# Kernel optimization log

Measured on AMD Instinct MI355X. Metric: run time of the kernel, lower is better.

The kernel has to match this reference:

```python
import jax, jax.numpy as jnp
import numpy as np

N = 8192          # total genes
B = 16            # number of ragged batch groups (equal-size here: 512 each)
D = 768           # hidden_dim
NEG = -1.0e9      # mask fill value used by the original module


def setup_inputs() -> dict:
    key = jax.random.key(0)
    ks = jax.random.split(key, 10)
    s = 0.02
    inp = {
        "gene_embeddings": jax.random.normal(ks[0], (N, D), dtype=jnp.float32),
        # sorted group ids: 16 contiguous groups of 512 genes
        "batch": (jnp.arange(N) // (N // B)).astype(jnp.int64),
        "Wq": jax.random.normal(ks[1], (D, D), dtype=jnp.float32) * s,
        "bq": jnp.zeros((D,), dtype=jnp.float32),
        "Wk": jax.random.normal(ks[2], (D, D), dtype=jnp.float32) * s,
        "bk": jnp.zeros((D,), dtype=jnp.float32),
        "Wv": jax.random.normal(ks[3], (D, D), dtype=jnp.float32) * s,
        "bv": jnp.zeros((D,), dtype=jnp.float32),
        "Wo": jax.random.normal(ks[4], (D, D), dtype=jnp.float32) * s,
        "bo": jnp.zeros((D,), dtype=jnp.float32),
        "beta": jnp.ones((1,), dtype=jnp.float32) * 0.1,
    }
    return inp


def reference(gene_embeddings, batch, Wq, bq, Wk, bk, Wv, bv, Wo, bo, beta):
    # Single-head attention over full hidden_dim (num_heads unused in original).
    x = gene_embeddings
    q = x @ Wq.T + bq                      # [N, D]
    k = x @ Wk.T + bk
    v = x @ Wv.T + bv
    scale = 1.0 / jnp.sqrt(jnp.asarray(D, dtype=x.dtype))
    scores = (q @ k.T) * scale             # [N, N]
    # block-diagonal group mask + diagonal self-mask (same -1e9 fill as torch code)
    same_group = batch[:, None] == batch[None, :]
    eye = jnp.eye(N, dtype=bool)
    allow = same_group & (~eye)
    scores = jnp.where(allow, scores, NEG)
    weights = jax.nn.softmax(scores, axis=-1)   # dropout in eval mode -> identity
    dyn = weights @ v                       # [N, D]
    dyn = dyn @ Wo.T + bo
    return x + beta * dyn
```

## Files before the change

### kernel.cpp

```cpp
#include <hip/hip_runtime.h>
#include <hip/hip_bf16.h>
#include <cstdint>

using u16 = unsigned short;
using u32 = unsigned int;

typedef __bf16 bf16x8 __attribute__((ext_vector_type(8)));
typedef float  f32x4  __attribute__((ext_vector_type(4)));

__device__ __forceinline__ u32 f2b2(float a, float b) {
    __hip_bfloat162 h = __float22bfloat162_rn(float2{a, b});
    u32 u;
    __builtin_memcpy(&u, &h, 4);
    return u;
}
__device__ __forceinline__ float b2f(u16 b) {
    u32 u = (u32)b << 16;
    float f;
    __builtin_memcpy(&f, &u, 4);
    return f;
}

__device__ __forceinline__ void gload_lds16(const u16* g, u16* l) {
    __builtin_amdgcn_global_load_lds(
        (const __attribute__((address_space(1))) void*)g,
        (__attribute__((address_space(3))) void*)l,
        16, 0, 0);
}

#define VMCNT(N)  asm volatile("s_waitcnt vmcnt(" #N ")" ::: "memory")
#define LGKMCNT0  asm volatile("s_waitcnt lgkmcnt(0)" ::: "memory")
#define BARRIER   asm volatile("s_barrier" ::: "memory")

__launch_bounds__(256)
__global__ void pack_kernel(const float* __restrict__ x,
                            const float* __restrict__ Wq,
                            const float* __restrict__ Wk,
                            const float* __restrict__ Wv,
                            const float* __restrict__ Wo,
                            const float* __restrict__ bq,
                            const float* __restrict__ bv,
                            const float* __restrict__ bo,
                            u16* __restrict__ xb,
                            u16* __restrict__ Wob,
                            u16* __restrict__ WqT,
                            u16* __restrict__ WkT,
                            u16* __restrict__ WvT,
                            float* __restrict__ czk,
                            float* __restrict__ bvoo)
{
    __shared__ u16 tl[64][72];
    const int b = blockIdx.x, tid = threadIdx.x;

    if (b < 3360) {
        int c = b * 256 + tid;
        long e = (long)c * 8;
        const float* src; u16* dst; long off;
        if (e < 6291456L) { src = x;  dst = xb;  off = e; }
        else              { src = Wo; dst = Wob; off = e - 6291456L; }
        float4 v0 = *(const float4*)(src + off);
        float4 v1 = *(const float4*)(src + off + 4);
        uint4 o;
        o.x = f2b2(v0.x, v0.y); o.y = f2b2(v0.z, v0.w);
        o.z = f2b2(v1.x, v1.y); o.w = f2b2(v1.z, v1.w);
        *(uint4*)(dst + off) = o;
    } else if (b < 3792) {
        int t = b - 3360;
        int w = t / 144, tt = t % 144;
        int tr = tt / 12, tc = tt % 12;
        const float* src0 = (w == 0) ? Wq : (w == 1) ? Wk : Wv;
        u16* dst0 = (w == 0) ? WqT : (w == 1) ? WkT : WvT;
        int lr = tid >> 2, lcb = (tid & 3) * 16;
        const float* src = src0 + (long)(tr * 64 + lr) * 768 + tc * 64 + lcb;
#pragma unroll
        for (int q = 0; q < 4; q++) {
            float4 v = *(const float4*)(src + q * 4);
            u32 p0 = f2b2(v.x, v.y), p1 = f2b2(v.z, v.w);
            tl[lr][lcb + q * 4 + 0] = (u16)p0;
            tl[lr][lcb + q * 4 + 1] = (u16)(p0 >> 16);
            tl[lr][lcb + q * 4 + 2] = (u16)p1;
            tl[lr][lcb + q * 4 + 3] = (u16)(p1 >> 16);
        }
        __syncthreads();
        int li = tid >> 2, lkb = (tid & 3) * 16;
        u16 o[16];
#pragma unroll
        for (int j = 0; j < 16; j++) o[j] = tl[lkb + j][li];
        u16* dst = dst0 + (long)(tc * 64 + li) * 768 + tr * 64 + lkb;
#pragma unroll
        for (int j = 0; j < 16; j++) dst[j] = o[j];
    } else if (b < 3984) {
        int wave = tid >> 6, lane = tid & 63;
        int j = (b - 3792) * 4 + wave;
        float acc = 0.f;
#pragma unroll
        for (int i = 0; i < 12; i++) {
            int rr = i * 64 + lane;
            acc += Wk[(long)rr * 768 + j] * bq[rr];
        }
#pragma unroll
        for (int d = 32; d; d >>= 1) acc += __shfl_xor(acc, d);
        if (lane == 0) czk[j] = acc;
    } else {
        int wave = tid >> 6, lane = tid & 63;
        int j = (b - 3984) * 4 + wave;
        float acc = 0.f;
#pragma unroll
        for (int i = 0; i < 12; i++) {
            int k = i * 64 + lane;
            acc += Wo[(long)j * 768 + k] * bv[k];
        }
#pragma unroll
        for (int d = 32; d; d >>= 1) acc += __shfl_xor(acc, d);
        if (lane == 0) bvoo[j] = acc + bo[j];
    }
}

template<int TM, int TN, int MODE>
__device__ __forceinline__ void gemm_body(
        const u16* __restrict__ A, int lda, long sAz,
        const u16* __restrict__ B, int ldb, long sBz,
        void* __restrict__ Cv, int ldc, long sCz,
        int K,
        const float* __restrict__ bias,
        float scale,
        u16* __restrict__ vTout)
{
    constexpr int FI = TM / 32;
    constexpr int FJ = TN / 32;
    constexpr int CA = TM / 64;
    constexpr int CB = TN / 64;

    __shared__ u16 As[2][TM * 32];
    __shared__ u16 Bs[2][TN * 32];

    const int tid  = threadIdx.x;
    const int g    = blockIdx.z;
    const u16* Ab = A + (long)g * sAz + (long)blockIdx.y * TM * lda;
    const u16* Bb = B + (long)g * sBz + (long)blockIdx.x * TN * ldb;

    const int wave = tid >> 6, lane = tid & 63;
    const int wm = (wave >> 1) * (TM / 2), wn = (wave & 1) * (TN / 2);
    const int ln15 = lane & 15, lq = lane >> 4;

    f32x4 acc[FI][FJ];
#pragma unroll
    for (int i = 0; i < FI; i++)
#pragma unroll
        for (int j = 0; j < FJ; j++)
            acc[i][j] = (f32x4){0.f, 0.f, 0.f, 0.f};

    const int srow = lane >> 2;
    const int sc   = ((lane & 3) ^ ((lane >> 4) & 3)) * 8;
    const u16* Ag[CA]; const u16* Bg[CB];
    int Al[CA], Bl[CB];
#pragma unroll
    for (int t = 0; t < CA; t++) {
        int c = wave * CA + t;
        Ag[t] = Ab + (long)(c * 16 + srow) * lda + sc;
        Al[t] = c * 512;
    }
#pragma unroll
    for (int t = 0; t < CB; t++) {
        int c = wave * CB + t;
        Bg[t] = Bb + (long)(c * 16 + srow) * ldb + sc;
        Bl[t] = c * 512;
    }

    const int foff = ln15 * 32 + ((lq ^ (ln15 >> 2)) * 8);
    const int nk = K >> 5;

#pragma unroll
    for (int t = 0; t < CA; t++) gload_lds16(Ag[t], &As[0][Al[t]]);
#pragma unroll
    for (int t = 0; t < CB; t++) gload_lds16(Bg[t], &Bs[0][Bl[t]]);

    for (int kt = 0; kt < nk; kt++) {
        const int cur = kt & 1;
        __syncthreads();
        if (kt + 1 < nk) {
            const int k0 = (kt + 1) * 32, nxt = cur ^ 1;
#pragma unroll
            for (int t = 0; t < CA; t++) gload_lds16(Ag[t] + k0, &As[nxt][Al[t]]);
#pragma unroll
            for (int t = 0; t < CB; t++) gload_lds16(Bg[t] + k0, &Bs[nxt][Bl[t]]);
        }

        bf16x8 af[FI], bfr[FJ];
#pragma unroll
        for (int i = 0; i < FI; i++)
            af[i] = *(const bf16x8*)&As[cur][(wm / 16 + i) * 512 + foff];
#pragma unroll
        for (int j = 0; j < FJ; j++)
            bfr[j] = *(const bf16x8*)&Bs[cur][(wn / 16 + j) * 512 + foff];
#pragma unroll
        for (int i = 0; i < FI; i++)
#pragma unroll
            for (int j = 0; j < FJ; j++)
                acc[i][j] = __builtin_amdgcn_mfma_f32_16x16x32_bf16(af[i], bfr[j], acc[i][j], 0, 0, 0);
    }

    const int baseRow = blockIdx.y * TM + wm;
    const int baseCol = blockIdx.x * TN + wn;

    if constexpr (MODE == 0) {
        if (baseCol < 768) {
            u16* C = (u16*)Cv;
#pragma unroll
            for (int i = 0; i < FI; i++)
#pragma unroll
                for (int j = 0; j < FJ; j++) {
                    int col = baseCol + j * 16 + ln15;
                    float bb = bias[col];
                    u32 p01 = f2b2(acc[i][j][0] + bb, acc[i][j][1] + bb);
                    u32 p23 = f2b2(acc[i][j][2] + bb, acc[i][j][3] + bb);
                    long r0 = (long)(baseRow + i * 16 + lq * 4) * ldc + col;
                    C[r0]           = (u16)p01;
                    C[r0 + ldc]     = (u16)(p01 >> 16);
                    C[r0 + 2 * ldc] = (u16)p23;
                    C[r0 + 3 * ldc] = (u16)(p23 >> 16);
                }
        } else {
#pragma unroll
            for (int i = 0; i < FI; i++)
#pragma unroll
                for (int j = 0; j < FJ; j++) {
                    int col = baseCol + j * 16 + ln15;
                    uint2 o;
                    o.x = f2b2(acc[i][j][0], acc[i][j][1]);
                    o.y = f2b2(acc[i][j][2], acc[i][j][3]);
                    *(uint2*)(vTout + (long)(col - 768) * 8192
                              + baseRow + i * 16 + lq * 4) = o;
                }
        }
    } else {
        u16* C = (u16*)Cv + (long)g * sCz;
#pragma unroll
        for (int i = 0; i < FI; i++)
#pragma unroll
            for (int j = 0; j < FJ; j++) {
                int col = baseCol + j * 16 + ln15;
                u32 p01 = f2b2(acc[i][j][0], acc[i][j][1]);
                u32 p23 = f2b2(acc[i][j][2], acc[i][j][3]);
                long r0 = (long)(baseRow + i * 16 + lq * 4) * ldc + col;
                C[r0]           = (u16)p01;
                C[r0 + ldc]     = (u16)(p01 >> 16);
                C[r0 + 2 * ldc] = (u16)p23;
                C[r0 + 3 * ldc] = (u16)(p23 >> 16);
            }
    }
}

__launch_bounds__(256)
__global__ void k_ww(const u16* WA, const u16* WB, void* WZplus)
{
    gemm_body<64, 128, 3>(WA, 768, 589824L, WB, 768, 589824L,
                          WZplus, 768, -589824L, 768,
                          nullptr, 0.f, nullptr);
}
__launch_bounds__(256)
__global__ void k_zv(const u16* A, const u16* B, void* C, const float* bias,
                     u16* vTout)
{
    gemm_body<128, 128, 0>(A, 768, 0, B, 768, 0, C, 768, 0, 768,
                           bias, 0.f, vTout);
}

__launch_bounds__(512)
__global__ void k_fattn(const u16* __restrict__ zbuf,
                        const u16* __restrict__ xb,
                        const u16* __restrict__ vwT,
                        float* __restrict__ out,
                        const float* __restrict__ bvoo,
                        const float* __restrict__ betaPtr,
                        float scale)
{
    __shared__ __align__(16) u16 smem[57344];
    u16* zl = smem;
    u16* xB = smem + 24576;
    u16* Pl = smem;
    float* redM = (float*)(smem + 16384);
    float* redS = (float*)(smem + 16640);
    u16* Vs = smem + 18432;

    const int bx = blockIdx.x;
    const int lg = ((bx & 7) << 5) + (bx >> 3);
    const int g = lg >> 4, rt = lg & 15;

    const int tid = threadIdx.x;
    const int wave = tid >> 6, lane = tid & 63;
    const int ln15 = lane & 15, lq = lane >> 4;
    const int srow = lane >> 2;
    const int sc = ((lane & 3) ^ ((lane >> 4) & 3)) * 8;
    const int foff = ln15 * 32 + ((lq ^ (ln15 >> 2)) * 8);

    const long rowBase = (long)(g * 512 + rt * 32);
    const u16* Zb = zbuf + rowBase * 768;
    const u16* Xg = xb + (long)g * 512 * 768;

    const int wm = (wave >> 2) * 16;
    const int wn = (wave & 3) * 128;

#pragma unroll
    for (int n = 0; n < 6; n++) {
        int cc = n * 8 + wave;
        gload_lds16(Zb + (long)((cc & 1) * 16 + srow) * 768 + (cc >> 1) * 32 + sc,
                    &zl[cc * 512]);
    }
    const u16* Bg[4]; int Bl[4];
#pragma unroll
    for (int t = 0; t < 4; t++) {
        int c = wave * 4 + t;
        Bg[t] = Xg + (long)(c * 16 + srow) * 768 + sc;
        Bl[t] = c * 512;
    }
#pragma unroll
    for (int t = 0; t < 4; t++) gload_lds16(Bg[t], &xB[Bl[t]]);
#pragma unroll
    for (int t = 0; t < 4; t++) gload_lds16(Bg[t] + 32, &xB[16384 + Bl[t]]);

    f32x4 acc[8];
#pragma unroll
    for (int j = 0; j < 8; j++) acc[j] = (f32x4){0.f, 0.f, 0.f, 0.f};

    for (int kt = 0; kt < 24; kt++) {
        const int cur = kt & 1;
        if (kt < 23) { VMCNT(4); } else { VMCNT(0); }
        BARRIER;
        bf16x8 af = *(const bf16x8*)&zl[(kt * 2 + (wm >> 4)) * 512 + foff];
        bf16x8 bfr[8];
#pragma unroll
        for (int j = 0; j < 8; j++)
            bfr[j] = *(const bf16x8*)&xB[cur * 16384 + (wn / 16 + j) * 512 + foff];
        LGKMCNT0;
        __builtin_amdgcn_sched_barrier(0);
        BARRIER;
        if (kt + 2 < 24) {
            const int k0 = (kt + 2) * 32;
#pragma unroll
            for (int t = 0; t < 4; t++)
                gload_lds16(Bg[t] + k0, &xB[cur * 16384 + Bl[t]]);
        }
        __builtin_amdgcn_s_setprio(1);
#pragma unroll
        for (int j = 0; j < 8; j++)
            acc[j] = __builtin_amdgcn_mfma_f32_16x16x32_bf16(af, bfr[j], acc[j], 0, 0, 0);
        __builtin_amdgcn_s_setprio(0);
    }

    __syncthreads();

#pragma unroll
    for (int sub = 0; sub < 4; sub++)
        gload_lds16(vwT + (long)(wave * 16 + srow) * 8192 + g * 512 + sub * 32 + sc,
                    &Vs[sub * 4096 + wave * 512]);
#pragma unroll
    for (int sub = 0; sub < 4; sub++)
        gload_lds16(vwT + (long)(wave * 16 + srow) * 8192 + g * 512 + 128 + sub * 32 + sc,
                    &Vs[16384 + sub * 4096 + wave * 512]);

    float mx[4];
#pragma unroll
    for (int rr = 0; rr < 4; rr++) mx[rr] = -3.0e38f;
#pragma unroll
    for (int j = 0; j < 8; j++)
#pragma unroll
        for (int rr = 0; rr < 4; rr++) {
            const int col = wn + j * 16 + ln15;
            float v = acc[j][rr] * scale;
            if (rt * 32 + wm + lq * 4 + rr == col) v = -1.0e9f;
            acc[j][rr] = v;
            mx[rr] = fmaxf(mx[rr], v);
        }
#pragma unroll
    for (int rr = 0; rr < 4; rr++) {
        mx[rr] = fmaxf(mx[rr], __shfl_xor(mx[rr], 1));
        mx[rr] = fmaxf(mx[rr], __shfl_xor(mx[rr], 2));
        mx[rr] = fmaxf(mx[rr], __shfl_xor(mx[rr], 4));
        mx[rr] = fmaxf(mx[rr], __shfl_xor(mx[rr], 8));
    }
    if (ln15 == 0) {
#pragma unroll
        for (int rr = 0; rr < 4; rr++)
            redM[(wm + lq * 4 + rr) * 4 + (wave & 3)] = mx[rr];
    }
    __syncthreads();

    float m[4], s[4];
#pragma unroll
    for (int rr = 0; rr < 4; rr++) {
        float4 rm = *(const float4*)&redM[(wm + lq * 4 + rr) * 4];
        m[rr] = fmaxf(fmaxf(rm.x, rm.y), fmaxf(rm.z, rm.w));
        s[rr] = 0.f;
    }
#pragma unroll
    for (int j = 0; j < 8; j++)
#pragma unroll
        for (int rr = 0; rr < 4; rr++) {
            float p = __expf(acc[j][rr] - m[rr]);
            acc[j][rr] = p;
            s[rr] += p;
        }
#pragma unroll
    for (int rr = 0; rr < 4; rr++) {
        s[rr] += __shfl_xor(s[rr], 1);
        s[rr] += __shfl_xor(s[rr], 2);
        s[rr] += __shfl_xor(s[rr], 4);
        s[rr] += __shfl_xor(s[rr], 8);
    }
    if (ln15 == 0) {
#pragma unroll
        for (int rr = 0; rr < 4; rr++)
            redS[(wm + lq * 4 + rr) * 4 + (wave & 3)] = s[rr];
    }
#pragma unroll
    for (int j = 0; j < 8; j++) {
        const int col = wn + j * 16 + ln15;
        const int c8 = col >> 3, b7 = col & 7;
#pragma unroll
        for (int rr = 0; rr < 4; rr++) {
            const int row = wm + lq * 4 + rr;
            Pl[(row * 64 + (c8 ^ (row & 7))) * 8 + b7] = (u16)f2b2(acc[j][rr], acc[j][rr]);
        }
    }
    __syncthreads();

    float invS[4];
#pragma unroll
    for (int rr = 0; rr < 4; rr++) {
        float4 rs = *(const float4*)&redS[(wm + lq * 4 + rr) * 4];
        invS[rr] = 1.0f / (rs.x + rs.y + rs.z + rs.w);
    }

    const int prow = wm + ln15;
    bf16x8 apr[16];
#pragma unroll
    for (int k4 = 0; k4 < 16; k4++)
        apr[k4] = *(const bf16x8*)&Pl[(prow * 64 + ((k4 * 4 + lq) ^ (prow & 7))) * 8];

    const int wnP = (wave & 3) * 32;
    f32x4 aP[6][2];
#pragma unroll
    for (int ct = 0; ct < 6; ct++) {
        aP[ct][0] = (f32x4){0.f, 0.f, 0.f, 0.f};
        aP[ct][1] = (f32x4){0.f, 0.f, 0.f, 0.f};
    }

#pragma unroll
    for (int ct = 0; ct < 6; ct++) {
#pragma unroll
        for (int kn2 = 0; kn2 < 4; kn2++) {
            const int ts = ct * 4 + kn2;
            const int cur = ts & 1;
            if (ts < 23) { VMCNT(4); } else { VMCNT(0); }
            BARRIER;
            bf16x8 b0[4], b1[4];
#pragma unroll
            for (int sub = 0; sub < 4; sub++) {
                b0[sub] = *(const bf16x8*)&Vs[cur * 16384 + sub * 4096
                                              + (wnP >> 4) * 512 + foff];
                b1[sub] = *(const bf16x8*)&Vs[cur * 16384 + sub * 4096
                                              + ((wnP >> 4) + 1) * 512 + foff];
            }
            LGKMCNT0;
            __builtin_amdgcn_sched_barrier(0);
            BARRIER;
            if (ts + 2 < 24) {
                const int tn = ts + 2, ctn = tn >> 2, kn = tn & 3;
#pragma unroll
                for (int sub = 0; sub < 4; sub++)
                    gload_lds16(vwT + (long)(ctn * 128 + wave * 16 + srow) * 8192
                                    + g * 512 + kn * 128 + sub * 32 + sc,
                                &Vs[cur * 16384 + sub * 4096 + wave * 512]);
            }
            __builtin_amdgcn_s_setprio(1);
#pragma unroll
            for (int sub = 0; sub < 4; sub++) {
                aP[ct][0] = __builtin_amdgcn_mfma_f32_16x16x32_bf16(apr[kn2 * 4 + sub], b0[sub], aP[ct][0], 0, 0, 0);
                aP[ct][1] = __builtin_amdgcn_mfma_f32_16x16x32_bf16(apr[kn2 * 4 + sub], b1[sub], aP[ct][1], 0, 0, 0);
            }
            __builtin_amdgcn_s_setprio(0);
        }
    }

    const float bet = betaPtr[0];
    const u16* Xr = xb + (rowBase + wm + lq * 4) * 768;
    float* O = out + (rowBase + wm + lq * 4) * 768;
#pragma unroll
    for (int ct = 0; ct < 6; ct++) {
#pragma unroll
        for (int jj = 0; jj < 2; jj++) {
            const int col = ct * 128 + wnP + jj * 16 + ln15;
            const float bb = bvoo[col];
#pragma unroll
            for (int rr = 0; rr < 4; rr++)
                O[rr * 768 + col] = b2f(Xr[rr * 768 + col])
                                    + bet * (invS[rr] * aP[ct][jj][rr] + bb);
        }
    }
}

extern "C" void kernel_launch(void* const* d_in, const int* in_sizes, int n_in,
                              void* d_out, int out_size, void* d_ws, size_t ws_size,
                              hipStream_t stream)
{
    const float* x    = (const float*)d_in[0];
    const float* Wq   = (const float*)d_in[2];
    const float* bq   = (const float*)d_in[3];
    const float* Wk   = (const float*)d_in[4];
    const float* bk   = (const float*)d_in[5];
    const float* Wv   = (const float*)d_in[6];
    const float* bv   = (const float*)d_in[7];
    const float* Wo   = (const float*)d_in[8];
    const float* bo   = (const float*)d_in[9];
    const float* beta = (const float*)d_in[10];
    float* out = (float*)d_out;
    (void)bk;

    char* ws = (char*)d_ws;
    u16*   zbuf = (u16*)(ws + 0);
    u16*   vwT  = (u16*)(ws + 12582912);
    u16*   xb   = (u16*)(ws + 25165824);
    u16*   WA   = (u16*)(ws + 46137344);
    u16*   WB   = (u16*)(ws + 48496640);
    u16*   WZ   = (u16*)(ws + 50855936);
    float* czk  = (float*)(ws + 53215232);
    float* bvoo = (float*)(ws + 53218304);

    u16* Wob = WA;
    u16* WkT = WA + 589824;
    u16* WvT = WB;
    u16* WqT = WB + 589824;

    const float scale = 0.03608439182435161f;

    pack_kernel<<<4176, 256, 0, stream>>>(x, Wq, Wk, Wv, Wo, bq, bv, bo,
                                          xb, Wob, WqT, WkT, WvT, czk, bvoo);

    k_ww<<<dim3(6, 12, 2), 256, 0, stream>>>(WA, WB, (void*)(WZ + 589824L));

    k_zv<<<dim3(12, 64, 1), 256, 0, stream>>>(xb, WZ, (void*)zbuf, czk, vwT);

    k_fattn<<<dim3(256), 512, 0, stream>>>(zbuf, xb, vwT, out, bvoo, beta,
                                           scale);
}
```

Measured before the change: 191.8 us.

## Give each wave private X tiles and triple-buffer V loads to drop barriers

```diff
diff --git a/kernel.cpp b/kernel.cpp
--- a/kernel.cpp
+++ b/kernel.cpp
@@ -280,7 +280,7 @@
     u16* xB = smem + 24576;
     u16* Pl = smem;
     float* redM = (float*)(smem + 16384);
-    float* redS = (float*)(smem + 16640);
+    float* redS = (float*)(smem + 16896);
     u16* Vs = smem + 18432;
 
     const int bx = blockIdx.x;
@@ -298,147 +298,172 @@
     const u16* Zb = zbuf + rowBase * 768;
     const u16* Xg = xb + (long)g * 512 * 768;
 
-    const int wm = (wave >> 2) * 16;
-    const int wn = (wave & 3) * 128;
-
 #pragma unroll
     for (int n = 0; n < 6; n++) {
         int cc = n * 8 + wave;
         gload_lds16(Zb + (long)((cc & 1) * 16 + srow) * 768 + (cc >> 1) * 32 + sc,
                     &zl[cc * 512]);
     }
-    const u16* Bg[4]; int Bl[4];
-#pragma unroll
-    for (int t = 0; t < 4; t++) {
-        int c = wave * 4 + t;
-        Bg[t] = Xg + (long)(c * 16 + srow) * 768 + sc;
-        Bl[t] = c * 512;
-    }
-#pragma unroll
-    for (int t = 0; t < 4; t++) gload_lds16(Bg[t], &xB[Bl[t]]);
-#pragma unroll
-    for (int t = 0; t < 4; t++) gload_lds16(Bg[t] + 32, &xB[16384 + Bl[t]]);
-
-    f32x4 acc[8];
-#pragma unroll
-    for (int j = 0; j < 8; j++) acc[j] = (f32x4){0.f, 0.f, 0.f, 0.f};
+    const u16* xsrc[4];
+#pragma unroll
+    for (int c = 0; c < 4; c++)
+        xsrc[c] = Xg + (long)(wave * 64 + c * 16 + srow) * 768 + sc;
+    u16* xd = xB + wave * 4096;
+#pragma unroll
+    for (int c = 0; c < 4; c++) gload_lds16(xsrc[c], &xd[c * 512]);
+#pragma unroll
+    for (int c = 0; c < 4; c++) gload_lds16(xsrc[c] + 32, &xd[2048 + c * 512]);
+
+    VMCNT(8);
+    BARRIER;
+
+    f32x4 acc[2][4];
+#pragma unroll
+    for (int mh = 0; mh < 2; mh++)
+#pragma unroll
+        for (int j = 0; j < 4; j++)
+            acc[mh][j] = (f32x4){0.f, 0.f, 0.f, 0.f};
 
     for (int kt = 0; kt < 24; kt++) {
         const int cur = kt & 1;
         if (kt < 23) { VMCNT(4); } else { VMCNT(0); }
-        BARRIER;
-        bf16x8 af = *(const bf16x8*)&zl[(kt * 2 + (wm >> 4)) * 512 + foff];
-        bf16x8 bfr[8];
-#pragma unroll
-        for (int j = 0; j < 8; j++)
-            bfr[j] = *(const bf16x8*)&xB[cur * 16384 + (wn / 16 + j) * 512 + foff];
+        bf16x8 af0 = *(const bf16x8*)&zl[(kt * 2 + 0) * 512 + foff];
+        bf16x8 af1 = *(const bf16x8*)&zl[(kt * 2 + 1) * 512 + foff];
+        bf16x8 bfr[4];
+#pragma unroll
+        for (int j = 0; j < 4; j++)
+            bfr[j] = *(const bf16x8*)&xd[cur * 2048 + j * 512 + foff];
         LGKMCNT0;
-        __builtin_amdgcn_sched_barrier(0);
-        BARRIER;
         if (kt + 2 < 24) {
             const int k0 = (kt + 2) * 32;
 #pragma unroll
-            for (int t = 0; t < 4; t++)
-                gload_lds16(Bg[t] + k0, &xB[cur * 16384 + Bl[t]]);
+            for (int c = 0; c < 4; c++)
+                gload_lds16(xsrc[c] + k0, &xd[cur * 2048 + c * 512]);
         }
         __builtin_amdgcn_s_setprio(1);
 #pragma unroll
-        for (int j = 0; j < 8; j++)
-            acc[j] = __builtin_amdgcn_mfma_f32_16x16x32_bf16(af, bfr[j], acc[j], 0, 0, 0);
+        for (int j = 0; j < 4; j++) {
+            acc[0][j] = __builtin_amdgcn_mfma_f32_16x16x32_bf16(af0, bfr[j], acc[0][j], 0, 0, 0);
+            acc[1][j] = __builtin_amdgcn_mfma_f32_16x16x32_bf16(af1, bfr[j], acc[1][j], 0, 0, 0);
+        }
         __builtin_amdgcn_s_setprio(0);
     }
 
     __syncthreads();
 
 #pragma unroll
-    for (int sub = 0; sub < 4; sub++)
+    for (int sub = 0; sub < 2; sub++)
         gload_lds16(vwT + (long)(wave * 16 + srow) * 8192 + g * 512 + sub * 32 + sc,
                     &Vs[sub * 4096 + wave * 512]);
 #pragma unroll
-    for (int sub = 0; sub < 4; sub++)
-        gload_lds16(vwT + (long)(wave * 16 + srow) * 8192 + g * 512 + 128 + sub * 32 + sc,
-                    &Vs[16384 + sub * 4096 + wave * 512]);
-
-    float mx[4];
-#pragma unroll
-    for (int rr = 0; rr < 4; rr++) mx[rr] = -3.0e38f;
-#pragma unroll
-    for (int j = 0; j < 8; j++)
+    for (int sub = 0; sub < 2; sub++)
+        gload_lds16(vwT + (long)(wave * 16 + srow) * 8192 + g * 512 + 64 + sub * 32 + sc,
+                    &Vs[8192 + sub * 4096 + wave * 512]);
+
+    float mx[2][4];
+#pragma unroll
+    for (int mh = 0; mh < 2; mh++)
+#pragma unroll
+        for (int rr = 0; rr < 4; rr++) mx[mh][rr] = -3.0e38f;
+#pragma unroll
+    for (int mh = 0; mh < 2; mh++)
+#pragma unroll
+        for (int j = 0; j < 4; j++)
+#pragma unroll
+            for (int rr = 0; rr < 4; rr++) {
+                const int col = wave * 64 + j * 16 + ln15;
+                float v = acc[mh][j][rr] * scale;
+                if (rt * 32 + mh * 16 + lq * 4 + rr == col) v = -1.0e9f;
+                acc[mh][j][rr] = v;
+                mx[mh][rr] = fmaxf(mx[mh][rr], v);
+            }
+#pragma unroll
+    for (int mh = 0; mh < 2; mh++)
 #pragma unroll
         for (int rr = 0; rr < 4; rr++) {
-            const int col = wn + j * 16 + ln15;
-            float v = acc[j][rr] * scale;
-            if (rt * 32 + wm + lq * 4 + rr == col) v = -1.0e9f;
-            acc[j][rr] = v;
-            mx[rr] = fmaxf(mx[rr], v);
-        }
+            mx[mh][rr] = fmaxf(mx[mh][rr], __shfl_xor(mx[mh][rr], 1));
+            mx[mh][rr] = fmaxf(mx[mh][rr], __shfl_xor(mx[mh][rr], 2));
+            mx[mh][rr] = fmaxf(mx[mh][rr], __shfl_xor(mx[mh][rr], 4));
+            mx[mh][rr] = fmaxf(mx[mh][rr], __shfl_xor(mx[mh][rr], 8));
+        }
+    if (ln15 == 0) {
+#pragma unroll
+        for (int mh = 0; mh < 2; mh++)
+#pragma unroll
+            for (int rr = 0; rr < 4; rr++)
+                redM[(mh * 16 + lq * 4 + rr) * 8 + wave] = mx[mh][rr];
+    }
+    __syncthreads();
+
+    float m_[2][4], s_[2][4];
+#pragma unroll
+    for (int mh = 0; mh < 2; mh++)
+#pragma unroll
+        for (int rr = 0; rr < 4; rr++) {
+            const int row = mh * 16 + lq * 4 + rr;
+            float4 a = *(const float4*)&redM[row * 8];
+            float4 b = *(const float4*)&redM[row * 8 + 4];
+            m_[mh][rr] = fmaxf(fmaxf(fmaxf(a.x, a.y), fmaxf(a.z, a.w)),
+                               fmaxf(fmaxf(b.x, b.y), fmaxf(b.z, b.w)));
+            s_[mh][rr] = 0.f;
+        }
+#pragma unroll
+    for (int mh = 0; mh < 2; mh++)
+#pragma unroll
+        for (int j = 0; j < 4; j++)
+#pragma unroll
+            for (int rr = 0; rr < 4; rr++) {
+                float p = __expf(acc[mh][j][rr] - m_[mh][rr]);
+                acc[mh][j][rr] = p;
+                s_[mh][rr] += p;
+            }
+#pragma unroll
+    for (int mh = 0; mh < 2; mh++)
+#pragma unroll
+        for (int rr = 0; rr < 4; rr++) {
+            s_[mh][rr] += __shfl_xor(s_[mh][rr], 1);
+            s_[mh][rr] += __shfl_xor(s_[mh][rr], 2);
+            s_[mh][rr] += __shfl_xor(s_[mh][rr], 4);
+            s_[mh][rr] += __shfl_xor(s_[mh][rr], 8);
+        }
+    if (ln15 == 0) {
+#pragma unroll
+        for (int mh = 0; mh < 2; mh++)
+#pragma unroll
+            for (int rr = 0; rr < 4; rr++)
+                redS[(mh * 16 + lq * 4 + rr) * 8 + wave] = s_[mh][rr];
+    }
+#pragma unroll
+    for (int mh = 0; mh < 2; mh++)
+#pragma unroll
+        for (int j = 0; j < 4; j++) {
+            const int col = wave * 64 + j * 16 + ln15;
+            const int c8 = col >> 3, b7 = col & 7;
+#pragma unroll
+            for (int rr = 0; rr < 4; rr++) {
+                const int row = mh * 16 + lq * 4 + rr;
+                Pl[(row * 64 + (c8 ^ (row & 7))) * 8 + b7] =
+                    (u16)f2b2(acc[mh][j][rr], acc[mh][j][rr]);
+            }
+        }
+    __syncthreads();
+
+    const int wm3 = (wave >> 2) * 16;
+    const int wnP = (wave & 3) * 32;
+    float invS[4];
 #pragma unroll
     for (int rr = 0; rr < 4; rr++) {
-        mx[rr] = fmaxf(mx[rr], __shfl_xor(mx[rr], 1));
-        mx[rr] = fmaxf(mx[rr], __shfl_xor(mx[rr], 2));
-        mx[rr] = fmaxf(mx[rr], __shfl_xor(mx[rr], 4));
-        mx[rr] = fmaxf(mx[rr], __shfl_xor(mx[rr], 8));
-    }
-    if (ln15 == 0) {
-#pragma unroll
-        for (int rr = 0; rr < 4; rr++)
-            redM[(wm + lq * 4 + rr) * 4 + (wave & 3)] = mx[rr];
-    }
-    __syncthreads();
-
-    float m[4], s[4];
-#pragma unroll
-    for (int rr = 0; rr < 4; rr++) {
-        float4 rm = *(const float4*)&redM[(wm + lq * 4 + rr) * 4];
-        m[rr] = fmaxf(fmaxf(rm.x, rm.y), fmaxf(rm.z, rm.w));
-        s[rr] = 0.f;
-    }
-#pragma unroll
-    for (int j = 0; j < 8; j++)
-#pragma unroll
-        for (int rr = 0; rr < 4; rr++) {
-            float p = __expf(acc[j][rr] - m[rr]);
-            acc[j][rr] = p;
-            s[rr] += p;
-        }
-#pragma unroll
-    for (int rr = 0; rr < 4; rr++) {
-        s[rr] += __shfl_xor(s[rr], 1);
-        s[rr] += __shfl_xor(s[rr], 2);
-        s[rr] += __shfl_xor(s[rr], 4);
-        s[rr] += __shfl_xor(s[rr], 8);
-    }
-    if (ln15 == 0) {
-#pragma unroll
-        for (int rr = 0; rr < 4; rr++)
-            redS[(wm + lq * 4 + rr) * 4 + (wave & 3)] = s[rr];
-    }
-#pragma unroll
-    for (int j = 0; j < 8; j++) {
-        const int col = wn + j * 16 + ln15;
-        const int c8 = col >> 3, b7 = col & 7;
-#pragma unroll
-        for (int rr = 0; rr < 4; rr++) {
-            const int row = wm + lq * 4 + rr;
-            Pl[(row * 64 + (c8 ^ (row & 7))) * 8 + b7] = (u16)f2b2(acc[j][rr], acc[j][rr]);
-        }
-    }
-    __syncthreads();
-
-    float invS[4];
-#pragma unroll
-    for (int rr = 0; rr < 4; rr++) {
-        float4 rs = *(const float4*)&redS[(wm + lq * 4 + rr) * 4];
-        invS[rr] = 1.0f / (rs.x + rs.y + rs.z + rs.w);
-    }
-
-    const int prow = wm + ln15;
+        const int row = wm3 + lq * 4 + rr;
+        float4 a = *(const float4*)&redS[row * 8];
+        float4 b = *(const float4*)&redS[row * 8 + 4];
+        invS[rr] = 1.0f / (a.x + a.y + a.z + a.w + b.x + b.y + b.z + b.w);
+    }
+    const int prow = wm3 + ln15;
     bf16x8 apr[16];
 #pragma unroll
     for (int k4 = 0; k4 < 16; k4++)
         apr[k4] = *(const bf16x8*)&Pl[(prow * 64 + ((k4 * 4 + lq) ^ (prow & 7))) * 8];
 
-    const int wnP = (wave & 3) * 32;
     f32x4 aP[6][2];
 #pragma unroll
     for (int ct = 0; ct < 6; ct++) {
@@ -449,43 +474,41 @@
 #pragma unroll
     for (int ct = 0; ct < 6; ct++) {
 #pragma unroll
-        for (int kn2 = 0; kn2 < 4; kn2++) {
-            const int ts = ct * 4 + kn2;
-            const int cur = ts & 1;
-            if (ts < 23) { VMCNT(4); } else { VMCNT(0); }
+        for (int kk = 0; kk < 8; kk++) {
+            const int ts = ct * 8 + kk;
+            const int cur = ts % 3;
+            if (ts < 47) { VMCNT(2); } else { VMCNT(0); }
             BARRIER;
-            bf16x8 b0[4], b1[4];
-#pragma unroll
-            for (int sub = 0; sub < 4; sub++) {
-                b0[sub] = *(const bf16x8*)&Vs[cur * 16384 + sub * 4096
+            bf16x8 b0[2], b1[2];
+#pragma unroll
+            for (int sub = 0; sub < 2; sub++) {
+                b0[sub] = *(const bf16x8*)&Vs[cur * 8192 + sub * 4096
                                               + (wnP >> 4) * 512 + foff];
-                b1[sub] = *(const bf16x8*)&Vs[cur * 16384 + sub * 4096
+                b1[sub] = *(const bf16x8*)&Vs[cur * 8192 + sub * 4096
                                               + ((wnP >> 4) + 1) * 512 + foff];
             }
-            LGKMCNT0;
-            __builtin_amdgcn_sched_barrier(0);
-            BARRIER;
-            if (ts + 2 < 24) {
-                const int tn = ts + 2, ctn = tn >> 2, kn = tn & 3;
-#pragma unroll
-                for (int sub = 0; sub < 4; sub++)
+            if (ts + 2 < 48) {
+                const int tn = ts + 2, ctn = tn >> 3, kkn = tn & 7;
+                const int nb = tn % 3;
+#pragma unroll
+                for (int sub = 0; sub < 2; sub++)
                     gload_lds16(vwT + (long)(ctn * 128 + wave * 16 + srow) * 8192
-                                    + g * 512 + kn * 128 + sub * 32 + sc,
-                                &Vs[cur * 16384 + sub * 4096 + wave * 512]);
+                                    + g * 512 + kkn * 64 + sub * 32 + sc,
+                                &Vs[nb * 8192 + sub * 4096 + wave * 512]);
             }
             __builtin_amdgcn_s_setprio(1);
 #pragma unroll
-            for (int sub = 0; sub < 4; sub++) {
-                aP[ct][0] = __builtin_amdgcn_mfma_f32_16x16x32_bf16(apr[kn2 * 4 + sub], b0[sub], aP[ct][0], 0, 0, 0);
-                aP[ct][1] = __builtin_amdgcn_mfma_f32_16x16x32_bf16(apr[kn2 * 4 + sub], b1[sub], aP[ct][1], 0, 0, 0);
+            for (int sub = 0; sub < 2; sub++) {
+                aP[ct][0] = __builtin_amdgcn_mfma_f32_16x16x32_bf16(apr[kk * 2 + sub], b0[sub], aP[ct][0], 0, 0, 0);
+                aP[ct][1] = __builtin_amdgcn_mfma_f32_16x16x32_bf16(apr[kk * 2 + sub], b1[sub], aP[ct][1], 0, 0, 0);
             }
             __builtin_amdgcn_s_setprio(0);
         }
     }
 
     const float bet = betaPtr[0];
-    const u16* Xr = xb + (rowBase + wm + lq * 4) * 768;
-    float* O = out + (rowBase + wm + lq * 4) * 768;
+    const u16* Xr = xb + (rowBase + wm3 + lq * 4) * 768;
+    float* O = out + (rowBase + wm3 + lq * 4) * 768;
 #pragma unroll
     for (int ct = 0; ct < 6; ct++) {
 #pragma unroll
```

After: 187.1 us. 2.5% less time.
